# Optimization experiments

Measured on AMD Instinct MI355X. Metric: run time of the kernel, lower is better.

## Reference

```python
import jax, jax.numpy as jnp
import numpy as np

N_NODES = 100000
N_EDGES = 1600000
N_GRAPHS = 64
D_IN = 128
D_HID = 128
D_OUT = 4
LEAKY_SLOPE = 0.01  # nn.LeakyReLU default


def setup_inputs() -> dict:
    key = jax.random.key(0)
    k1, k2, k3, k4, k5 = jax.random.split(key, 5)
    x = jax.random.normal(k1, (N_NODES, D_IN), dtype=jnp.float32)
    edge_index = jax.random.randint(k2, (2, N_EDGES), 0, N_NODES, dtype=jnp.int32)
    batch = jnp.sort(jax.random.randint(k3, (N_NODES,), 0, N_GRAPHS, dtype=jnp.int32))
    s1 = 1.0 / np.sqrt(D_IN)
    W1 = jax.random.uniform(k4, (D_IN, D_HID), jnp.float32, -s1, s1)
    b1 = jnp.zeros((D_HID,), jnp.float32)
    W2 = jax.random.uniform(k5, (D_HID, D_OUT), jnp.float32, -s1, s1)
    b2 = jnp.zeros((D_OUT,), jnp.float32)
    return {"x": x, "edge_index": edge_index, "batch": batch,
            "W1": W1, "b1": b1, "W2": W2, "b2": b2}


def _gcn_conv(x, src, dst, norm, W, b, n_nodes):
    # h = X W; messages = norm * h[src]; aggregate at dst; add bias
    h = x @ W
    msg = h[src] * norm[:, None]
    agg = jax.ops.segment_sum(msg, dst, num_segments=n_nodes)
    return agg + b


def reference(x, edge_index, batch, W1, b1, W2, b2):
    n = x.shape[0]
    # add self-loops (PyG GCNConv default)
    loops = jnp.arange(n, dtype=edge_index.dtype)
    src = jnp.concatenate([edge_index[0], loops])
    dst = jnp.concatenate([edge_index[1], loops])
    # symmetric normalization: deg over target index, weight 1
    deg = jax.ops.segment_sum(jnp.ones_like(src, dtype=x.dtype), dst, num_segments=n)
    deg_is = jnp.where(deg > 0, jax.lax.rsqrt(deg), 0.0)
    norm = deg_is[src] * deg_is[dst]

    h = _gcn_conv(x, src, dst, norm, W1, b1, n)
    h = jnp.where(h >= 0, h, LEAKY_SLOPE * h)  # LeakyReLU
    # dropout is identity at inference
    h = _gcn_conv(h, src, dst, norm, W2, b2, n)

    # global mean pool over graphs
    sums = jax.ops.segment_sum(h, batch, num_segments=N_GRAPHS)
    cnts = jax.ops.segment_sum(jnp.ones((n,), h.dtype), batch, num_segments=N_GRAPHS)
    pooled = sums / jnp.maximum(cnts, 1.0)[:, None]
    return jax.nn.softmax(pooled, axis=1)
```

## Files before the change

### kernel.cpp

```cpp
#include <hip/hip_runtime.h>

#define D 128
#define NG 64
#define NPB 256
#define MAXBK 512
#define CAPB 8192
#define PCHUNK 2048
#define PLCAP 5376
#define LDA 136

typedef unsigned int uint;
typedef unsigned short ushort_t;
typedef unsigned char uchar_t;
typedef float v2f __attribute__((ext_vector_type(2)));
typedef short s8v __attribute__((ext_vector_type(8)));
typedef float f4v __attribute__((ext_vector_type(4)));

__device__ __forceinline__ uint bfr(float x) {
    uint u = __float_as_uint(x);
    return (u + 0x7FFFu + ((u >> 16) & 1u)) >> 16;
}

__global__ __launch_bounds__(256) void k_init(const float* __restrict__ W,
                                              short* __restrict__ W1T,
                                              int* __restrict__ gcur,
                                              float* __restrict__ psum,
                                              float* __restrict__ pcnt, int NBK) {
    int tid = threadIdx.x;
    int idx = blockIdx.x * 256 + tid;
    int nn = idx >> 7, kk = idx & 127;
    W1T[idx] = (short)bfr(W[kk * D + nn]);
    if (idx < NBK) gcur[idx] = idx * CAPB;
    if (blockIdx.x == 0) {
        psum[tid] = 0.f;
        if (tid < NG) pcnt[tid] = 0.f;
    }
}

__global__ __launch_bounds__(256) void k_part(const int* __restrict__ edge,
                                              int* __restrict__ gcur, int* __restrict__ p1,
                                              int E, int NBK) {
    __shared__ int hist[MAXBK], scn[MAXBK], curb[MAXBK], fixb[MAXBK];
    __shared__ int ps[256];
    __shared__ int sortb[PCHUNK];
    __shared__ ushort_t sbkt[PCHUNK];
    int tid = threadIdx.x;
    for (int i = tid; i < MAXBK; i += 256) { hist[i] = 0; curb[i] = 0; }
    __syncthreads();
    int lo = blockIdx.x * PCHUNK;
    int hi = min(lo + PCHUNK, E);
    int cnt = hi - lo;
    int4 dv[2], sv[2];
#pragma unroll
    for (int it = 0; it < 2; ++it) {
        int q = lo + tid * 4 + it * 1024;
        if (q + 4 <= hi) {
            dv[it] = *(const int4*)&edge[E + q];
            sv[it] = *(const int4*)&edge[q];
            atomicAdd(&hist[dv[it].x >> 8], 1);
            atomicAdd(&hist[dv[it].y >> 8], 1);
            atomicAdd(&hist[dv[it].z >> 8], 1);
            atomicAdd(&hist[dv[it].w >> 8], 1);
        } else {
            dv[it].x = (q + 0 < hi) ? edge[E + q + 0] : 0;
            dv[it].y = (q + 1 < hi) ? edge[E + q + 1] : 0;
            dv[it].z = (q + 2 < hi) ? edge[E + q + 2] : 0;
            dv[it].w = 0;
            sv[it].x = (q + 0 < hi) ? edge[q + 0] : 0;
            sv[it].y = (q + 1 < hi) ? edge[q + 1] : 0;
            sv[it].z = (q + 2 < hi) ? edge[q + 2] : 0;
            sv[it].w = 0;
            if (q + 0 < hi) atomicAdd(&hist[dv[it].x >> 8], 1);
            if (q + 1 < hi) atomicAdd(&hist[dv[it].y >> 8], 1);
            if (q + 2 < hi) atomicAdd(&hist[dv[it].z >> 8], 1);
        }
    }
    __syncthreads();
    int a = hist[2 * tid], b = hist[2 * tid + 1];
    ps[tid] = a + b;
    __syncthreads();
    for (int o = 1; o < 256; o <<= 1) {
        int x = (tid >= o) ? ps[tid - o] : 0;
        __syncthreads();
        ps[tid] += x;
        __syncthreads();
    }
    int pe = ps[tid] - (a + b);
    scn[2 * tid] = pe;
    scn[2 * tid + 1] = pe + a;
    __syncthreads();
    for (int bk = tid; bk < NBK; bk += 256)
        if (hist[bk]) fixb[bk] = atomicAdd(&gcur[bk], hist[bk]) - scn[bk];
    __syncthreads();
#pragma unroll
    for (int it = 0; it < 2; ++it) {
        int q = lo + tid * 4 + it * 1024;
        {
            int d2 = dv[it].x, s = sv[it].x;
            if (q + 0 < hi) {
                int bk = d2 >> 8;
                int r = scn[bk] + atomicAdd(&curb[bk], 1);
                sortb[r] = ((d2 & 255) << 17) | s;
                sbkt[r] = (ushort_t)bk;
            }
        }
        {
            int d2 = dv[it].y, s = sv[it].y;
            if (q + 1 < hi) {
                int bk = d2 >> 8;
                int r = scn[bk] + atomicAdd(&curb[bk], 1);
                sortb[r] = ((d2 & 255) << 17) | s;
                sbkt[r] = (ushort_t)bk;
            }
        }
        {
            int d2 = dv[it].z, s = sv[it].z;
            if (q + 2 < hi) {
                int bk = d2 >> 8;
                int r = scn[bk] + atomicAdd(&curb[bk], 1);
                sortb[r] = ((d2 & 255) << 17) | s;
                sbkt[r] = (ushort_t)bk;
            }
        }
        {
            int d2 = dv[it].w, s = sv[it].w;
            if (q + 3 < hi) {
                int bk = d2 >> 8;
                int r = scn[bk] + atomicAdd(&curb[bk], 1);
                sortb[r] = ((d2 & 255) << 17) | s;
                sbkt[r] = (ushort_t)bk;
            }
        }
    }
    __syncthreads();
    for (int p = tid; p < cnt; p += 256) {
        int bk = sbkt[p];
        p1[fixb[bk] + p] = sortb[p];
    }
}

__global__ __launch_bounds__(512) void k_place(const int* __restrict__ p1,
                                               const int* __restrict__ gcur,
                                               int* __restrict__ ed, int2* __restrict__ offdeg,
                                               float* __restrict__ dinv, int n) {
    __shared__ int cnts[256], scn[256], cur[256];
    __shared__ int outb[PLCAP];
    __shared__ int tot;
    int tid = threadIdx.x;
    int b = blockIdx.x;
    int base = b * CAPB;
    int cnt = gcur[b] - base;
    int end = base + cnt;
    int node0 = b << 8;
    if (tid < 256) { cnts[tid] = 0; cur[tid] = 0; }
    __syncthreads();
    int4 ev[4];
#pragma unroll
    for (int it = 0; it < 4; ++it) {
        int q = base + tid * 4 + it * 2048;
        ev[it] = *(const int4*)&p1[q];
        if (q + 4 <= end) {
            atomicAdd(&cnts[ev[it].x >> 17], 1);
            atomicAdd(&cnts[ev[it].y >> 17], 1);
            atomicAdd(&cnts[ev[it].z >> 17], 1);
            atomicAdd(&cnts[ev[it].w >> 17], 1);
        } else if (q < end) {
            atomicAdd(&cnts[ev[it].x >> 17], 1);
            if (q + 1 < end) atomicAdd(&cnts[ev[it].y >> 17], 1);
            if (q + 2 < end) atomicAdd(&cnts[ev[it].z >> 17], 1);
        }
    }
    __syncthreads();
    int v0 = 0, pc = 0;
    if (tid < 256) {
        v0 = cnts[tid];
        pc = (v0 + 3) & ~3;
        scn[tid] = pc;
    }
    __syncthreads();
    for (int o = 1; o < 256; o <<= 1) {
        int x = 0;
        if (tid < 256 && tid >= o) x = scn[tid - o];
        __syncthreads();
        if (tid < 256) scn[tid] += x;
        __syncthreads();
    }
    if (tid == 255) tot = scn[255];
    if (tid < 256) {
        int excl = scn[tid] - pc;
        int node = node0 + tid;
        if (node < n) {
            offdeg[node] = make_int2(base + excl, v0);
            dinv[node] = rsqrtf((float)(v0 + 1));
        }
    }
    __syncthreads();
    if (tid < 256) scn[tid] -= pc;
    __syncthreads();
#pragma unroll
    for (int it = 0; it < 4; ++it) {
        int q = base + tid * 4 + it * 2048;
        {
            int v = ev[it].x;
            if (q + 0 < end) {
                int l = v >> 17;
                int r = scn[l] + atomicAdd(&cur[l], 1);
                if (r < PLCAP) outb[r] = v & 0x1FFFF; else ed[base + r] = v & 0x1FFFF;
            }
        }
        {
            int v = ev[it].y;
            if (q + 1 < end) {
                int l = v >> 17;
                int r = scn[l] + atomicAdd(&cur[l], 1);
                if (r < PLCAP) outb[r] = v & 0x1FFFF; else ed[base + r] = v & 0x1FFFF;
            }
        }
        {
            int v = ev[it].z;
            if (q + 2 < end) {
                int l = v >> 17;
                int r = scn[l] + atomicAdd(&cur[l], 1);
                if (r < PLCAP) outb[r] = v & 0x1FFFF; else ed[base + r] = v & 0x1FFFF;
            }
        }
        {
            int v = ev[it].w;
            if (q + 3 < end) {
                int l = v >> 17;
                int r = scn[l] + atomicAdd(&cur[l], 1);
                if (r < PLCAP) outb[r] = v & 0x1FFFF; else ed[base + r] = v & 0x1FFFF;
            }
        }
    }
    __syncthreads();
    int lim = (tot < PLCAP) ? tot : PLCAP;
    for (int p = tid; p < lim; p += 512) ed[base + p] = outb[p];
}

__global__ __launch_bounds__(256) void k_gemm_mfma(const float* __restrict__ X,
                                                   const short* __restrict__ W1T,
                                                   const float* __restrict__ dinv,
                                                   uchar_t* __restrict__ H8b, int M) {
    __shared__ short sA[128 * LDA];
    __shared__ short sB[128 * LDA];
    __shared__ float sDinv[128];
    const int tid = threadIdx.x;
    const int blockM = blockIdx.x * 128;

    if (tid < 128) {
        int gm = blockM + tid;
        sDinv[tid] = (gm < M) ? dinv[gm] : 0.f;
    }
    {
        int c = tid & 31, g = tid >> 5;
#pragma unroll
        for (int i = 0; i < 16; ++i) {
            int r = g + i * 8;
            int gm = blockM + r;
            float4 v = make_float4(0, 0, 0, 0);
            if (gm < M) v = *(const float4*)&X[(size_t)gm * D + c * 4];
            uint lo = bfr(v.x) | (bfr(v.y) << 16);
            uint hi = bfr(v.z) | (bfr(v.w) << 16);
            *(uint2*)&sA[r * LDA + c * 4] = make_uint2(lo, hi);
        }
    }
    {
        int nn = tid >> 1, seg = tid & 1;
        const short* src = W1T + nn * 128 + seg * 64;
        short* dst = &sB[nn * LDA + seg * 64];
#pragma unroll
        for (int i = 0; i < 8; ++i)
            *(int4*)&dst[i * 8] = *(const int4*)&src[i * 8];
    }
    __syncthreads();

    const int wv = tid >> 6;
    const int lane = tid & 63;
    const int m0w = (wv >> 1) * 64, n0w = (wv & 1) * 64;
    const int mrow = lane & 15;
    const int quad = lane >> 4;

    f4v acc[4][4];
#pragma unroll
    for (int mi = 0; mi < 4; ++mi)
#pragma unroll
        for (int ni = 0; ni < 4; ++ni) acc[mi][ni] = (f4v)(0.f);

#pragma unroll
    for (int ks = 0; ks < 4; ++ks) {
        s8v af[4], bf[4];
#pragma unroll
        for (int mi = 0; mi < 4; ++mi)
            af[mi] = *(const s8v*)&sA[(m0w + mi * 16 + mrow) * LDA + ks * 32 + quad * 8];
#pragma unroll
        for (int ni = 0; ni < 4; ++ni)
            bf[ni] = *(const s8v*)&sB[(n0w + ni * 16 + mrow) * LDA + ks * 32 + quad * 8];
#pragma unroll
        for (int mi = 0; mi < 4; ++mi)
#pragma unroll
            for (int ni = 0; ni < 4; ++ni)
                acc[mi][ni] = __builtin_amdgcn_mfma_f32_16x16x32_bf16(af[mi], bf[ni], acc[mi][ni], 0, 0, 0);
    }

#pragma unroll
    for (int mi = 0; mi < 4; ++mi) {
#pragma unroll
        for (int r = 0; r < 4; ++r) {
            int lrow = m0w + mi * 16 + quad * 4 + r;
            int gm = blockM + lrow;
            if (gm >= M) continue;
            float di = sDinv[lrow];
#pragma unroll
            for (int ni = 0; ni < 4; ++ni) {
                int col = n0w + ni * 16 + mrow;
                float v = acc[mi][ni][r] * di;
                uint p = __builtin_amdgcn_cvt_pk_fp8_f32(v, v, 0u, false);
                H8b[(size_t)gm * 128 + col] = (uchar_t)(p & 0xFF);
            }
        }
    }
}

__device__ __forceinline__ void acc4(float& c0, float& c1, float& c2, float& c3, uint r) {
    v2f lo = __builtin_amdgcn_cvt_pk_f32_fp8(r, false);
    v2f hi = __builtin_amdgcn_cvt_pk_f32_fp8(r, true);
    c0 += lo.x; c1 += lo.y; c2 += hi.x; c3 += hi.y;
}

__global__ __launch_bounds__(256, 8) void k_gather(const uint* __restrict__ T,
                                                   const int2* __restrict__ offdeg,
                                                   const int* __restrict__ ed,
                                                   const float* __restrict__ dinv,
                                                   const float* __restrict__ b1,
                                                   const float* __restrict__ W2,
                                                   float4* __restrict__ zs,
                                                   int n) {
    int tid = threadIdx.x;
    int node = blockIdx.x * 8 + (tid >> 5);
    if (node >= n) return;
    int lane = tid & 31;
    const uint* Tl = T + lane;
    float di = dinv[node];
    float c0, c1, c2, c3;
    {
        uint h = Tl[node << 5];
        v2f lo = __builtin_amdgcn_cvt_pk_f32_fp8(h, false);
        v2f hi = __builtin_amdgcn_cvt_pk_f32_fp8(h, true);
        c0 = lo.x; c1 = lo.y; c2 = hi.x; c3 = hi.y;
    }
    int2 od = offdeg[node];
    int j = od.x, j1 = od.x + od.y;
    for (; j + 16 <= j1; j += 16) {
        int4 e0 = *(const int4*)&ed[j];
        int4 e1 = *(const int4*)&ed[j + 4];
        int4 e2 = *(const int4*)&ed[j + 8];
        int4 e3 = *(const int4*)&ed[j + 12];
        uint r0 = Tl[e0.x << 5], r1 = Tl[e0.y << 5], r2 = Tl[e0.z << 5], r3 = Tl[e0.w << 5];
        uint r4 = Tl[e1.x << 5], r5 = Tl[e1.y << 5], r6 = Tl[e1.z << 5], r7 = Tl[e1.w << 5];
        uint r8 = Tl[e2.x << 5], r9 = Tl[e2.y << 5], r10 = Tl[e2.z << 5], r11 = Tl[e2.w << 5];
        uint r12 = Tl[e3.x << 5], r13 = Tl[e3.y << 5], r14 = Tl[e3.z << 5], r15 = Tl[e3.w << 5];
        acc4(c0, c1, c2, c3, r0);  acc4(c0, c1, c2, c3, r1);
        acc4(c0, c1, c2, c3, r2);  acc4(c0, c1, c2, c3, r3);
        acc4(c0, c1, c2, c3, r4);  acc4(c0, c1, c2, c3, r5);
        acc4(c0, c1, c2, c3, r6);  acc4(c0, c1, c2, c3, r7);
        acc4(c0, c1, c2, c3, r8);  acc4(c0, c1, c2, c3, r9);
        acc4(c0, c1, c2, c3, r10); acc4(c0, c1, c2, c3, r11);
        acc4(c0, c1, c2, c3, r12); acc4(c0, c1, c2, c3, r13);
        acc4(c0, c1, c2, c3, r14); acc4(c0, c1, c2, c3, r15);
    }
    if (j + 8 <= j1) {
        int4 e0 = *(const int4*)&ed[j];
        int4 e1 = *(const int4*)&ed[j + 4];
        uint r0 = Tl[e0.x << 5], r1 = Tl[e0.y << 5], r2 = Tl[e0.z << 5], r3 = Tl[e0.w << 5];
        uint r4 = Tl[e1.x << 5], r5 = Tl[e1.y << 5], r6 = Tl[e1.z << 5], r7 = Tl[e1.w << 5];
        acc4(c0, c1, c2, c3, r0); acc4(c0, c1, c2, c3, r1);
        acc4(c0, c1, c2, c3, r2); acc4(c0, c1, c2, c3, r3);
        acc4(c0, c1, c2, c3, r4); acc4(c0, c1, c2, c3, r5);
        acc4(c0, c1, c2, c3, r6); acc4(c0, c1, c2, c3, r7);
        j += 8;
    }
    if (j + 4 <= j1) {
        int4 e0 = *(const int4*)&ed[j];
        uint r0 = Tl[e0.x << 5], r1 = Tl[e0.y << 5], r2 = Tl[e0.z << 5], r3 = Tl[e0.w << 5];
        acc4(c0, c1, c2, c3, r0); acc4(c0, c1, c2, c3, r1);
        acc4(c0, c1, c2, c3, r2); acc4(c0, c1, c2, c3, r3);
        j += 4;
    }
    for (; j < j1; ++j) {
        uint r = Tl[ed[j] << 5];
        acc4(c0, c1, c2, c3, r);
    }
    int f = lane * 4;
    float v0 = di * c0 + b1[f + 0];
    float v1 = di * c1 + b1[f + 1];
    float v2 = di * c2 + b1[f + 2];
    float v3 = di * c3 + b1[f + 3];
    v0 = v0 >= 0.f ? v0 : 0.01f * v0;
    v1 = v1 >= 0.f ? v1 : 0.01f * v1;
    v2 = v2 >= 0.f ? v2 : 0.01f * v2;
    v3 = v3 >= 0.f ? v3 : 0.01f * v3;
    const float4* W2v = (const float4*)W2;
    float4 w0 = W2v[f + 0], w1 = W2v[f + 1], w2 = W2v[f + 2], w3 = W2v[f + 3];
    float a0 = v0 * w0.x + v1 * w1.x + v2 * w2.x + v3 * w3.x;
    float a1 = v0 * w0.y + v1 * w1.y + v2 * w2.y + v3 * w3.y;
    float a2 = v0 * w0.z + v1 * w1.z + v2 * w2.z + v3 * w3.z;
    float a3 = v0 * w0.w + v1 * w1.w + v2 * w2.w + v3 * w3.w;
#pragma unroll
    for (int o = 16; o >= 1; o >>= 1) {
        a0 += __shfl_xor(a0, o);
        a1 += __shfl_xor(a1, o);
        a2 += __shfl_xor(a2, o);
        a3 += __shfl_xor(a3, o);
    }
    if (lane == 0) zs[node] = make_float4(di * a0, di * a1, di * a2, di * a3);
}

__global__ __launch_bounds__(256) void k_pool2(const int* __restrict__ p1,
                                               const int* __restrict__ gcur,
                                               const float4* __restrict__ zs,
                                               const float* __restrict__ dinv,
                                               const int* __restrict__ batch,
                                               float* __restrict__ psum, float* __restrict__ pcnt,
                                               int n) {
    __shared__ float ls[NG * 4];
    __shared__ float lc[NG];
    __shared__ float dinvd[NPB];
    __shared__ int gl[NPB];
    int tid = threadIdx.x;
    int b = blockIdx.x >> 1;
    int half = blockIdx.x & 1;
    int node0 = b << 8;
    int node = node0 + tid;
    ls[tid] = 0.f;
    if (tid < NG) lc[tid] = 0.f;
    bool valid = node < n;
    float di = valid ? dinv[node] : 0.f;
    int g = valid ? batch[node] : -1;
    dinvd[tid] = di;
    gl[tid] = g;
    __syncthreads();
    float a0 = 0.f, a1 = 0.f, a2 = 0.f, a3 = 0.f;
    int cg = -1;
    auto PROC = [&](int v, float4 zv) {
        int dl = v >> 17;
        float w = dinvd[dl];
        int eg = gl[dl];
        if (eg != cg) {
            if (cg >= 0) {
                atomicAdd(&ls[cg * 4 + 0], a0);
                atomicAdd(&ls[cg * 4 + 1], a1);
                atomicAdd(&ls[cg * 4 + 2], a2);
                atomicAdd(&ls[cg * 4 + 3], a3);
            }
            cg = eg;
            a0 = a1 = a2 = a3 = 0.f;
        }
        a0 += w * zv.x; a1 += w * zv.y; a2 += w * zv.z; a3 += w * zv.w;
    };
    if (half == 0 && valid) {
        float4 zv = zs[node];
        cg = g;
        a0 = di * zv.x; a1 = di * zv.y; a2 = di * zv.z; a3 = di * zv.w;
        atomicAdd(&lc[g], 1.f);
    }
    int base = b * CAPB;
    int cnt = gcur[b] - base;
    int mid = (cnt >> 1) & ~3;
    int s0 = base + (half ? mid : 0);
    int s1 = base + (half ? cnt : mid);
    int p0 = s0 + tid * 4;
    for (; p0 + 4 <= s1; p0 += 1024) {
        int4 vv = *(const int4*)&p1[p0];
        float4 zb0 = zs[vv.x & 0x1FFFF];
        float4 zb1 = zs[vv.y & 0x1FFFF];
        float4 zb2 = zs[vv.z & 0x1FFFF];
        float4 zb3 = zs[vv.w & 0x1FFFF];
        PROC(vv.x, zb0); PROC(vv.y, zb1); PROC(vv.z, zb2); PROC(vv.w, zb3);
    }
    for (; p0 < s1; ++p0) {
        int v = p1[p0];
        PROC(v, zs[v & 0x1FFFF]);
    }
    if (cg >= 0) {
        atomicAdd(&ls[cg * 4 + 0], a0);
        atomicAdd(&ls[cg * 4 + 1], a1);
        atomicAdd(&ls[cg * 4 + 2], a2);
        atomicAdd(&ls[cg * 4 + 3], a3);
    }
    __syncthreads();
    atomicAdd(&psum[tid], ls[tid]);
    if (tid < NG) atomicAdd(&pcnt[tid], lc[tid]);
}

__global__ void k_final(const float* __restrict__ psum, const float* __restrict__ pcnt,
                        const float* __restrict__ b2, float* __restrict__ out) {
    int g = threadIdx.x;
    float c = fmaxf(pcnt[g], 1.f);
    float inv = 1.f / c;
    float l0 = psum[g * 4 + 0] * inv + b2[0];
    float l1 = psum[g * 4 + 1] * inv + b2[1];
    float l2 = psum[g * 4 + 2] * inv + b2[2];
    float l3 = psum[g * 4 + 3] * inv + b2[3];
    float m = fmaxf(fmaxf(l0, l1), fmaxf(l2, l3));
    float e0 = expf(l0 - m), e1 = expf(l1 - m), e2 = expf(l2 - m), e3 = expf(l3 - m);
    float s = 1.f / (e0 + e1 + e2 + e3);
    *(float4*)&out[g * 4] = make_float4(e0 * s, e1 * s, e2 * s, e3 * s);
}

extern "C" void kernel_launch(void* const* d_in, const int* in_sizes, int n_in,
                              void* d_out, int out_size, void* d_ws, size_t ws_size,
                              hipStream_t stream) {
    const float* X = (const float*)d_in[0];
    const int* edge = (const int*)d_in[1];
    const int* batch = (const int*)d_in[2];
    const float* W1 = (const float*)d_in[3];
    const float* b1 = (const float*)d_in[4];
    const float* W2 = (const float*)d_in[5];
    const float* b2 = (const float*)d_in[6];
    float* out = (float*)d_out;
    const int n = in_sizes[2];
    const int E = in_sizes[1] / 2;
    const int NBK = (n + NPB - 1) / NPB;

    uint* Hs = (uint*)d_ws;
    int* p1 = (int*)(Hs + (size_t)n * 32);
    int* ed = p1 + (size_t)NBK * CAPB;
    float4* zs = (float4*)(ed + (size_t)NBK * CAPB);
    float* dinv = (float*)(zs + n);
    int2* offdeg = (int2*)(dinv + n);
    short* W1T = (short*)(offdeg + n);
    int* gcur = (int*)(W1T + 16384);
    float* psum = (float*)(gcur + MAXBK);
    float* pcnt = psum + NG * 4;

    const int NP = (E + PCHUNK - 1) / PCHUNK;
    const int NGB = (n + 7) / 8;

    k_init<<<64, 256, 0, stream>>>(W1, W1T, gcur, psum, pcnt, NBK);
    k_part<<<NP, 256, 0, stream>>>(edge, gcur, p1, E, NBK);
    k_place<<<NBK, 512, 0, stream>>>(p1, gcur, ed, offdeg, dinv, n);

    k_gemm_mfma<<<(n + 127) / 128, 256, 0, stream>>>(X, W1T, dinv, (uchar_t*)Hs, n);

    k_gather<<<NGB, 256, 0, stream>>>(Hs, offdeg, ed, dinv, b1, W2, zs, n);

    k_pool2<<<NBK * 2, 256, 0, stream>>>(p1, gcur, zs, dinv, batch, psum, pcnt, n);
    k_final<<<1, 64, 0, stream>>>(psum, pcnt, b2, out);
}
```

Measured before the change: 224.9 us.

## Halve node buckets and pool second layer via per-node CSR gather

```diff
diff --git a/kernel.cpp b/kernel.cpp
--- a/kernel.cpp
+++ b/kernel.cpp
@@ -2,11 +2,11 @@
 
 #define D 128
 #define NG 64
-#define NPB 256
-#define MAXBK 512
-#define CAPB 8192
+#define NPB 128
+#define MAXBK 1024
+#define CAPB 4096
 #define PCHUNK 2048
-#define PLCAP 5376
+#define PLCAP 4608
 #define LDA 136
 
 typedef unsigned int uint;
@@ -57,10 +57,10 @@
         if (q + 4 <= hi) {
             dv[it] = *(const int4*)&edge[E + q];
             sv[it] = *(const int4*)&edge[q];
-            atomicAdd(&hist[dv[it].x >> 8], 1);
-            atomicAdd(&hist[dv[it].y >> 8], 1);
-            atomicAdd(&hist[dv[it].z >> 8], 1);
-            atomicAdd(&hist[dv[it].w >> 8], 1);
+            atomicAdd(&hist[dv[it].x >> 7], 1);
+            atomicAdd(&hist[dv[it].y >> 7], 1);
+            atomicAdd(&hist[dv[it].z >> 7], 1);
+            atomicAdd(&hist[dv[it].w >> 7], 1);
         } else {
             dv[it].x = (q + 0 < hi) ? edge[E + q + 0] : 0;
             dv[it].y = (q + 1 < hi) ? edge[E + q + 1] : 0;
@@ -70,14 +70,16 @@
             sv[it].y = (q + 1 < hi) ? edge[q + 1] : 0;
             sv[it].z = (q + 2 < hi) ? edge[q + 2] : 0;
             sv[it].w = 0;
-            if (q + 0 < hi) atomicAdd(&hist[dv[it].x >> 8], 1);
-            if (q + 1 < hi) atomicAdd(&hist[dv[it].y >> 8], 1);
-            if (q + 2 < hi) atomicAdd(&hist[dv[it].z >> 8], 1);
-        }
-    }
-    __syncthreads();
-    int a = hist[2 * tid], b = hist[2 * tid + 1];
-    ps[tid] = a + b;
+            if (q + 0 < hi) atomicAdd(&hist[dv[it].x >> 7], 1);
+            if (q + 1 < hi) atomicAdd(&hist[dv[it].y >> 7], 1);
+            if (q + 2 < hi) atomicAdd(&hist[dv[it].z >> 7], 1);
+        }
+    }
+    __syncthreads();
+    int a = hist[4 * tid + 0], b = hist[4 * tid + 1];
+    int c = hist[4 * tid + 2], d = hist[4 * tid + 3];
+    int s4 = a + b + c + d;
+    ps[tid] = s4;
     __syncthreads();
     for (int o = 1; o < 256; o <<= 1) {
         int x = (tid >= o) ? ps[tid - o] : 0;
@@ -85,9 +87,11 @@
         ps[tid] += x;
         __syncthreads();
     }
-    int pe = ps[tid] - (a + b);
-    scn[2 * tid] = pe;
-    scn[2 * tid + 1] = pe + a;
+    int pe = ps[tid] - s4;
+    scn[4 * tid + 0] = pe;
+    scn[4 * tid + 1] = pe + a;
+    scn[4 * tid + 2] = pe + a + b;
+    scn[4 * tid + 3] = pe + a + b + c;
     __syncthreads();
     for (int bk = tid; bk < NBK; bk += 256)
         if (hist[bk]) fixb[bk] = atomicAdd(&gcur[bk], hist[bk]) - scn[bk];
@@ -98,36 +102,36 @@
         {
             int d2 = dv[it].x, s = sv[it].x;
             if (q + 0 < hi) {
-                int bk = d2 >> 8;
+                int bk = d2 >> 7;
                 int r = scn[bk] + atomicAdd(&curb[bk], 1);
-                sortb[r] = ((d2 & 255) << 17) | s;
+                sortb[r] = ((d2 & 127) << 17) | s;
                 sbkt[r] = (ushort_t)bk;
             }
         }
         {
             int d2 = dv[it].y, s = sv[it].y;
             if (q + 1 < hi) {
-                int bk = d2 >> 8;
+                int bk = d2 >> 7;
                 int r = scn[bk] + atomicAdd(&curb[bk], 1);
-                sortb[r] = ((d2 & 255) << 17) | s;
+                sortb[r] = ((d2 & 127) << 17) | s;
                 sbkt[r] = (ushort_t)bk;
             }
         }
         {
             int d2 = dv[it].z, s = sv[it].z;
             if (q + 2 < hi) {
-                int bk = d2 >> 8;
+                int bk = d2 >> 7;
                 int r = scn[bk] + atomicAdd(&curb[bk], 1);
-                sortb[r] = ((d2 & 255) << 17) | s;
+                sortb[r] = ((d2 & 127) << 17) | s;
                 sbkt[r] = (ushort_t)bk;
             }
         }
         {
             int d2 = dv[it].w, s = sv[it].w;
             if (q + 3 < hi) {
-                int bk = d2 >> 8;
+                int bk = d2 >> 7;
                 int r = scn[bk] + atomicAdd(&curb[bk], 1);
-                sortb[r] = ((d2 & 255) << 17) | s;
+                sortb[r] = ((d2 & 127) << 17) | s;
                 sbkt[r] = (ushort_t)bk;
             }
         }
@@ -139,11 +143,11 @@
     }
 }
 
-__global__ __launch_bounds__(512) void k_place(const int* __restrict__ p1,
+__global__ __launch_bounds__(256) void k_place(const int* __restrict__ p1,
                                                const int* __restrict__ gcur,
                                                int* __restrict__ ed, int2* __restrict__ offdeg,
                                                float* __restrict__ dinv, int n) {
-    __shared__ int cnts[256], scn[256], cur[256];
+    __shared__ int cnts[NPB], scn[NPB], cur[NPB];
     __shared__ int outb[PLCAP];
     __shared__ int tot;
     int tid = threadIdx.x;
@@ -151,13 +155,13 @@
     int base = b * CAPB;
     int cnt = gcur[b] - base;
     int end = base + cnt;
-    int node0 = b << 8;
-    if (tid < 256) { cnts[tid] = 0; cur[tid] = 0; }
+    int node0 = b << 7;
+    if (tid < NPB) { cnts[tid] = 0; cur[tid] = 0; }
     __syncthreads();
     int4 ev[4];
 #pragma unroll
     for (int it = 0; it < 4; ++it) {
-        int q = base + tid * 4 + it * 2048;
+        int q = base + tid * 4 + it * 1024;
         ev[it] = *(const int4*)&p1[q];
         if (q + 4 <= end) {
             atomicAdd(&cnts[ev[it].x >> 17], 1);
@@ -172,40 +176,39 @@
     }
     __syncthreads();
     int v0 = 0, pc = 0;
-    if (tid < 256) {
+    if (tid < NPB) {
         v0 = cnts[tid];
         pc = (v0 + 3) & ~3;
         scn[tid] = pc;
     }
     __syncthreads();
-    for (int o = 1; o < 256; o <<= 1) {
+    for (int o = 1; o < NPB; o <<= 1) {
         int x = 0;
-        if (tid < 256 && tid >= o) x = scn[tid - o];
+        if (tid < NPB && tid >= o) x = scn[tid - o];
         __syncthreads();
-        if (tid < 256) scn[tid] += x;
+        if (tid < NPB) scn[tid] += x;
         __syncthreads();
     }
-    if (tid == 255) tot = scn[255];
-    if (tid < 256) {
+    if (tid == NPB - 1) tot = scn[NPB - 1];
+    if (tid < NPB) {
         int excl = scn[tid] - pc;
         int node = node0 + tid;
         if (node < n) {
             offdeg[node] = make_int2(base + excl, v0);
             dinv[node] = rsqrtf((float)(v0 + 1));
         }
-    }
-    __syncthreads();
-    if (tid < 256) scn[tid] -= pc;
+        scn[tid] = excl;
+    }
     __syncthreads();
 #pragma unroll
     for (int it = 0; it < 4; ++it) {
-        int q = base + tid * 4 + it * 2048;
+        int q = base + tid * 4 + it * 1024;
         {
             int v = ev[it].x;
             if (q + 0 < end) {
                 int l = v >> 17;
                 int r = scn[l] + atomicAdd(&cur[l], 1);
-                if (r < PLCAP) outb[r] = v & 0x1FFFF; else ed[base + r] = v & 0x1FFFF;
+                if (r < PLCAP) outb[r] = v & 0x1FFFF;
             }
         }
         {
@@ -213,7 +216,7 @@
             if (q + 1 < end) {
                 int l = v >> 17;
                 int r = scn[l] + atomicAdd(&cur[l], 1);
-                if (r < PLCAP) outb[r] = v & 0x1FFFF; else ed[base + r] = v & 0x1FFFF;
+                if (r < PLCAP) outb[r] = v & 0x1FFFF;
             }
         }
         {
@@ -221,7 +224,7 @@
             if (q + 2 < end) {
                 int l = v >> 17;
                 int r = scn[l] + atomicAdd(&cur[l], 1);
-                if (r < PLCAP) outb[r] = v & 0x1FFFF; else ed[base + r] = v & 0x1FFFF;
+                if (r < PLCAP) outb[r] = v & 0x1FFFF;
             }
         }
         {
@@ -229,13 +232,13 @@
             if (q + 3 < end) {
                 int l = v >> 17;
                 int r = scn[l] + atomicAdd(&cur[l], 1);
-                if (r < PLCAP) outb[r] = v & 0x1FFFF; else ed[base + r] = v & 0x1FFFF;
+                if (r < PLCAP) outb[r] = v & 0x1FFFF;
             }
         }
     }
     __syncthreads();
     int lim = (tot < PLCAP) ? tot : PLCAP;
-    for (int p = tid; p < lim; p += 512) ed[base + p] = outb[p];
+    for (int p = tid; p < lim; p += 256) ed[base + p] = outb[p];
 }
 
 __global__ __launch_bounds__(256) void k_gemm_mfma(const float* __restrict__ X,
@@ -416,8 +419,8 @@
     if (lane == 0) zs[node] = make_float4(di * a0, di * a1, di * a2, di * a3);
 }
 
-__global__ __launch_bounds__(256) void k_pool2(const int* __restrict__ p1,
-                                               const int* __restrict__ gcur,
+__global__ __launch_bounds__(256) void k_pool2(const int2* __restrict__ offdeg,
+                                               const int* __restrict__ ed,
                                                const float4* __restrict__ zs,
                                                const float* __restrict__ dinv,
                                                const int* __restrict__ batch,
@@ -425,68 +428,46 @@
                                                int n) {
     __shared__ float ls[NG * 4];
     __shared__ float lc[NG];
-    __shared__ float dinvd[NPB];
-    __shared__ int gl[NPB];
     int tid = threadIdx.x;
-    int b = blockIdx.x >> 1;
-    int half = blockIdx.x & 1;
-    int node0 = b << 8;
-    int node = node0 + tid;
     ls[tid] = 0.f;
     if (tid < NG) lc[tid] = 0.f;
-    bool valid = node < n;
-    float di = valid ? dinv[node] : 0.f;
-    int g = valid ? batch[node] : -1;
-    dinvd[tid] = di;
-    gl[tid] = g;
-    __syncthreads();
-    float a0 = 0.f, a1 = 0.f, a2 = 0.f, a3 = 0.f;
-    int cg = -1;
-    auto PROC = [&](int v, float4 zv) {
-        int dl = v >> 17;
-        float w = dinvd[dl];
-        int eg = gl[dl];
-        if (eg != cg) {
-            if (cg >= 0) {
-                atomicAdd(&ls[cg * 4 + 0], a0);
-                atomicAdd(&ls[cg * 4 + 1], a1);
-                atomicAdd(&ls[cg * 4 + 2], a2);
-                atomicAdd(&ls[cg * 4 + 3], a3);
-            }
-            cg = eg;
-            a0 = a1 = a2 = a3 = 0.f;
-        }
-        a0 += w * zv.x; a1 += w * zv.y; a2 += w * zv.z; a3 += w * zv.w;
-    };
-    if (half == 0 && valid) {
-        float4 zv = zs[node];
-        cg = g;
-        a0 = di * zv.x; a1 = di * zv.y; a2 = di * zv.z; a3 = di * zv.w;
-        atomicAdd(&lc[g], 1.f);
-    }
-    int base = b * CAPB;
-    int cnt = gcur[b] - base;
-    int mid = (cnt >> 1) & ~3;
-    int s0 = base + (half ? mid : 0);
-    int s1 = base + (half ? cnt : mid);
-    int p0 = s0 + tid * 4;
-    for (; p0 + 4 <= s1; p0 += 1024) {
-        int4 vv = *(const int4*)&p1[p0];
-        float4 zb0 = zs[vv.x & 0x1FFFF];
-        float4 zb1 = zs[vv.y & 0x1FFFF];
-        float4 zb2 = zs[vv.z & 0x1FFFF];
-        float4 zb3 = zs[vv.w & 0x1FFFF];
-        PROC(vv.x, zb0); PROC(vv.y, zb1); PROC(vv.z, zb2); PROC(vv.w, zb3);
-    }
-    for (; p0 < s1; ++p0) {
-        int v = p1[p0];
-        PROC(v, zs[v & 0x1FFFF]);
-    }
-    if (cg >= 0) {
-        atomicAdd(&ls[cg * 4 + 0], a0);
-        atomicAdd(&ls[cg * 4 + 1], a1);
-        atomicAdd(&ls[cg * 4 + 2], a2);
-        atomicAdd(&ls[cg * 4 + 3], a3);
+    __syncthreads();
+    int idx = blockIdx.x * 256 + tid;
+    int node = idx >> 1, h = idx & 1;
+    if (node < n) {
+        int2 od = offdeg[node];
+        int d = od.y;
+        int qend = od.x + (d & ~3);
+        float a0 = 0.f, a1 = 0.f, a2 = 0.f, a3 = 0.f;
+        if (h == 0) {
+            float4 z = zs[node];
+            a0 = z.x; a1 = z.y; a2 = z.z; a3 = z.w;
+            for (int j = qend; j < od.x + d; ++j) {
+                float4 z2 = zs[ed[j]];
+                a0 += z2.x; a1 += z2.y; a2 += z2.z; a3 += z2.w;
+            }
+        }
+        for (int j = od.x + h * 4; j + 4 <= qend; j += 8) {
+            int4 e = *(const int4*)&ed[j];
+            float4 z0 = zs[e.x], z1 = zs[e.y], z2 = zs[e.z], z3 = zs[e.w];
+            a0 += z0.x + z1.x + z2.x + z3.x;
+            a1 += z0.y + z1.y + z2.y + z3.y;
+            a2 += z0.z + z1.z + z2.z + z3.z;
+            a3 += z0.w + z1.w + z2.w + z3.w;
+        }
+        a0 += __shfl_xor(a0, 1);
+        a1 += __shfl_xor(a1, 1);
+        a2 += __shfl_xor(a2, 1);
+        a3 += __shfl_xor(a3, 1);
+        if (h == 0) {
+            float di = dinv[node];
+            int g = batch[node];
+            atomicAdd(&ls[g * 4 + 0], di * a0);
+            atomicAdd(&ls[g * 4 + 1], di * a1);
+            atomicAdd(&ls[g * 4 + 2], di * a2);
+            atomicAdd(&ls[g * 4 + 3], di * a3);
+            atomicAdd(&lc[g], 1.f);
+        }
     }
     __syncthreads();
     atomicAdd(&psum[tid], ls[tid]);
@@ -536,15 +517,16 @@
 
     const int NP = (E + PCHUNK - 1) / PCHUNK;
     const int NGB = (n + 7) / 8;
+    const int NPOOL = (2 * n + 255) / 256;
 
     k_init<<<64, 256, 0, stream>>>(W1, W1T, gcur, psum, pcnt, NBK);
     k_part<<<NP, 256, 0, stream>>>(edge, gcur, p1, E, NBK);
-    k_place<<<NBK, 512, 0, stream>>>(p1, gcur, ed, offdeg, dinv, n);
+    k_place<<<NBK, 256, 0, stream>>>(p1, gcur, ed, offdeg, dinv, n);
 
     k_gemm_mfma<<<(n + 127) / 128, 256, 0, stream>>>(X, W1T, dinv, (uchar_t*)Hs, n);
 
     k_gather<<<NGB, 256, 0, stream>>>(Hs, offdeg, ed, dinv, b1, W2, zs, n);
 
-    k_pool2<<<NBK * 2, 256, 0, stream>>>(p1, gcur, zs, dinv, batch, psum, pcnt, n);
+    k_pool2<<<NPOOL, 256, 0, stream>>>(offdeg, ed, zs, dinv, batch, psum, pcnt, n);
     k_final<<<1, 64, 0, stream>>>(psum, pcnt, b2, out);
 }
```

Result: slower. 233.9 us (+4.0%).
